# Kernel tuning notes

Hardware: AMD Instinct MI355X
Metric: run time of the kernel (lower is better)

## Reference

```python
import jax, jax.numpy as jnp
import numpy as np

EMBED = 256      # input_size
DOWN = 64        # expert hidden_size
NUM_EXPERTS = 10
TOPK = 2
GATE_SCALE = 0.5
LOSS_COEF = 1.0
CV_EPS = 1e-10


def setup_inputs() -> dict:
    key = jax.random.key(0)
    ks = jax.random.split(key, 6)
    B, N = 16, 4096
    x = jax.random.normal(ks[0], (B, N, EMBED), jnp.float32)
    # gating weight (Parameter in torch; random here so top-k is non-degenerate)
    w_gate = jax.random.normal(ks[1], (EMBED, NUM_EXPERTS), jnp.float32) * 0.02
    # expert MLP params: fc1 (EMBED->DOWN), relu, fc2 (DOWN->EMBED)
    w1 = jax.random.normal(ks[2], (NUM_EXPERTS, EMBED, DOWN), jnp.float32) * (1.0 / np.sqrt(EMBED))
    b1 = jnp.zeros((NUM_EXPERTS, DOWN), jnp.float32)
    w2 = jax.random.normal(ks[3], (NUM_EXPERTS, DOWN, EMBED), jnp.float32) * (1.0 / np.sqrt(DOWN))
    b2 = jnp.zeros((NUM_EXPERTS, EMBED), jnp.float32)
    return {"x": x, "w_gate": w_gate, "w1": w1, "b1": b1, "w2": w2, "b2": b2}


def _cv_squared(v):
    # torch: x.var() / (x.mean()**2 + eps), unbiased variance
    return jnp.var(v, ddof=1) / (jnp.mean(v) ** 2 + CV_EPS)


def reference(x, w_gate, w1, b1, w2, b2):
    B, N, D = x.shape
    xt = x.reshape(B * N, D)                      # (T, D)
    T = B * N

    # --- noisy top-k gating (eval mode: no noise) ---
    logits = xt @ w_gate                          # (T, E)
    top_logits, top_idx = jax.lax.top_k(logits, TOPK)
    top_gates = jax.nn.softmax(top_logits, axis=-1)
    gates = jnp.zeros((T, NUM_EXPERTS), x.dtype).at[
        jnp.arange(T)[:, None], top_idx].set(top_gates)   # (T, E), sparse rows

    importance = gates.sum(axis=0)                               # (E,)
    load = jnp.sum(gates > 0, axis=0).astype(x.dtype)            # (E,)
    aux_loss = (_cv_squared(importance) + _cv_squared(load)) * LOSS_COEF

    # --- expert FFN dispatch+combine (dense equivalent: zero gates kill terms) ---
    h = jax.nn.relu(jnp.einsum('td,edh->teh', xt, w1) + b1[None])   # (T, E, DOWN)
    ye = jnp.einsum('teh,eho->teo', h, w2) + b2[None]               # (T, E, D)
    y = jnp.einsum('te,teo->to', gates, ye)                         # (T, D)

    out = y.reshape(B, N, -1)
    # self-KD L1 loss vs zeros, computed BEFORE gate_scale is applied
    kd_loss = jnp.mean(jnp.abs(out))
    moe_loss = aux_loss + kd_loss
    return out * GATE_SCALE, moe_loss
```

## Files before the change

kernel.cpp:

```cpp
#include <hip/hip_runtime.h>
#include <hip/hip_bf16.h>

#define T_TOKENS 65536
#define EMBED 256
#define DOWN 64
#define NE 10
#define TILE 64
#define XROW 72

typedef __attribute__((ext_vector_type(8))) short short8;
typedef __attribute__((ext_vector_type(4))) float f32x4;

__device__ inline unsigned short f2bf(float f) {
    unsigned u = __builtin_bit_cast(unsigned, f);
    u += 0x7fff + ((u >> 16) & 1);
    return (unsigned short)(u >> 16);
}
__device__ inline float bf2f(unsigned short h) {
    unsigned u = ((unsigned)h) << 16;
    return __builtin_bit_cast(float, u);
}

__global__ __launch_bounds__(256) void pack_kernel(
    const float* __restrict__ w1, const float* __restrict__ w2,
    unsigned short* __restrict__ w1ph, unsigned short* __restrict__ w1pl,
    unsigned short* __restrict__ w2ph, unsigned short* __restrict__ w2pl)
{
    int gid = blockIdx.x * 256 + threadIdx.x;
    int lane = gid & 63;
    int fid = gid >> 6;
    int n16 = lane & 15;
    int kbase = ((lane >> 4) & 3) * 8;
    if (fid < 320) {
        int kb = fid & 7, ect = fid >> 3;
        int ct = ect & 3, e = ect >> 2;
        int n = ct * 16 + n16;
        int k0 = kb * 32 + kbase;
#pragma unroll
        for (int j = 0; j < 8; ++j) {
            float v = w1[((size_t)e * EMBED + k0 + j) * DOWN + n];
            unsigned short h = f2bf(v);
            w1ph[(size_t)fid * 512 + lane * 8 + j] = h;
            w1pl[(size_t)fid * 512 + lane * 8 + j] = f2bf(v - bf2f(h));
        }
    } else if (fid < 640) {
        int f2 = fid - 320;
        int kb = f2 & 1, ect = f2 >> 1;
        int ct = ect & 15, e = ect >> 4;
        int n = ct * 16 + n16;
        int k0 = kb * 32 + kbase;
#pragma unroll
        for (int j = 0; j < 8; ++j) {
            float v = w2[((size_t)e * DOWN + k0 + j) * EMBED + n];
            unsigned short h = f2bf(v);
            w2ph[(size_t)f2 * 512 + lane * 8 + j] = h;
            w2pl[(size_t)f2 * 512 + lane * 8 + j] = f2bf(v - bf2f(h));
        }
    }
}

__global__ __launch_bounds__(256) void gating_kernel(
    const float* __restrict__ x, const float* __restrict__ wg,
    int* __restrict__ counts, float* __restrict__ importance,
    int* __restrict__ tok_list, float* __restrict__ gate_list)
{
    __shared__ int lcount[NE];
    __shared__ float limp[NE];
    __shared__ int gbase[NE];
    int tid = threadIdx.x;
    if (tid < NE) { lcount[tid] = 0; limp[tid] = 0.f; }
    __syncthreads();

    int t = blockIdx.x * 256 + tid;
    float acc[NE];
#pragma unroll
    for (int e = 0; e < NE; e++) acc[e] = 0.f;
    const float4* x4 = (const float4*)(x + (size_t)t * EMBED);
    for (int d4 = 0; d4 < EMBED / 4; d4++) {
        float4 xv = x4[d4];
        const float* xs = (const float*)&xv;
#pragma unroll
        for (int j = 0; j < 4; j++) {
            int d = d4 * 4 + j;
#pragma unroll
            for (int e = 0; e < NE; e++)
                acc[e] = fmaf(xs[j], wg[d * NE + e], acc[e]);
        }
    }
    float l0 = -INFINITY, l1 = -INFINITY;
    int i0 = 0, i1 = 0;
#pragma unroll
    for (int e = 0; e < NE; e++) {
        float v = acc[e];
        if (v > l0) { l1 = l0; i1 = i0; l0 = v; i0 = e; }
        else if (v > l1) { l1 = v; i1 = e; }
    }
    float ex = __expf(l1 - l0);
    float g0 = 1.f / (1.f + ex);
    float g1 = ex * g0;

    int lp0 = atomicAdd(&lcount[i0], 1);
    int lp1 = atomicAdd(&lcount[i1], 1);
    atomicAdd(&limp[i0], g0);
    atomicAdd(&limp[i1], g1);
    __syncthreads();
    if (tid < NE) {
        gbase[tid] = atomicAdd(&counts[tid], lcount[tid]);
        atomicAdd(&importance[tid], limp[tid]);
    }
    __syncthreads();
    int p0 = gbase[i0] + lp0;
    int p1 = gbase[i1] + lp1;
    tok_list[i0 * T_TOKENS + p0] = (t << 1) | 0;
    gate_list[i0 * T_TOKENS + p0] = g0;
    tok_list[i1 * T_TOKENS + p1] = (t << 1) | 1;
    gate_list[i1 * T_TOKENS + p1] = g1;
}

__global__ __launch_bounds__(256, 4) void expert_kernel(
    const float* __restrict__ x,
    const unsigned short* __restrict__ w1ph, const unsigned short* __restrict__ w1pl,
    const unsigned short* __restrict__ w2ph, const unsigned short* __restrict__ w2pl,
    const float* __restrict__ b1, const float* __restrict__ b2,
    const int* __restrict__ counts,
    const int* __restrict__ tok_list, const float* __restrict__ gate_list,
    float* __restrict__ y0, float* __restrict__ y1)
{
    int e = blockIdx.y;
    int cnt = counts[e];
    int start = blockIdx.x * TILE;
    if (start >= cnt) return;
    int m = min(TILE, cnt - start);

    __shared__ __align__(16) unsigned short Xh[TILE * XROW];
    __shared__ __align__(16) unsigned short Xl[TILE * XROW];
    __shared__ __align__(16) unsigned short Hh[TILE * XROW];
    __shared__ __align__(16) unsigned short Hl[TILE * XROW];
    __shared__ int toks[TILE];
    __shared__ float gval[TILE];

    int tid = threadIdx.x;
    if (tid < TILE) {
        int v = 0; float g = 0.f;
        if (tid < m) {
            v = tok_list[e * T_TOKENS + start + tid];
            g = gate_list[e * T_TOKENS + start + tid];
        }
        toks[tid] = v; gval[tid] = g;
    }
    __syncthreads();

    int lane = tid & 63;
    int wv = tid >> 6;
    int ln15 = lane & 15;
    int quad = lane >> 4;

    int srow = tid >> 2;
    int scol0 = (tid & 3) * 16;
    bool srow_ok = srow < m;
    const float* xrow = x + (size_t)(toks[srow] >> 1) * EMBED;

    f32x4 acc1[4];
#pragma unroll
    for (int rt = 0; rt < 4; ++rt) acc1[rt] = (f32x4){0.f, 0.f, 0.f, 0.f};

    const unsigned short* w1he = w1ph + (((size_t)e * 4 + wv) * 8) * 512;
    const unsigned short* w1le = w1pl + (((size_t)e * 4 + wv) * 8) * 512;

    for (int c = 0; c < 4; ++c) {
#pragma unroll
        for (int p = 0; p < 4; ++p) {
            int col = scol0 + p * 4;
            float4 v = make_float4(0.f, 0.f, 0.f, 0.f);
            if (srow_ok) v = *(const float4*)(xrow + c * 64 + col);
            const float* vs = (const float*)&v;
            ushort4 hv, lv;
            unsigned short* hp = (unsigned short*)&hv;
            unsigned short* lp = (unsigned short*)&lv;
#pragma unroll
            for (int i = 0; i < 4; ++i) {
                unsigned short h = f2bf(vs[i]);
                hp[i] = h;
                lp[i] = f2bf(vs[i] - bf2f(h));
            }
            *(ushort4*)&Xh[srow * XROW + col] = hv;
            *(ushort4*)&Xl[srow * XROW + col] = lv;
        }
        __syncthreads();
#pragma unroll
        for (int kb = 0; kb < 2; ++kb) {
            int kbg = c * 2 + kb;
            short8 bh = *(const short8*)(w1he + (size_t)kbg * 512 + lane * 8);
            short8 bl = *(const short8*)(w1le + (size_t)kbg * 512 + lane * 8);
            int aoff = kb * 32 + quad * 8;
#pragma unroll
            for (int rt = 0; rt < 4; ++rt) {
                short8 ah = *(const short8*)&Xh[(rt * 16 + ln15) * XROW + aoff];
                short8 al = *(const short8*)&Xl[(rt * 16 + ln15) * XROW + aoff];
                acc1[rt] = __builtin_amdgcn_mfma_f32_16x16x32_bf16(ah, bh, acc1[rt], 0, 0, 0);
                acc1[rt] = __builtin_amdgcn_mfma_f32_16x16x32_bf16(ah, bl, acc1[rt], 0, 0, 0);
                acc1[rt] = __builtin_amdgcn_mfma_f32_16x16x32_bf16(al, bh, acc1[rt], 0, 0, 0);
            }
        }
        __syncthreads();
    }

    float b1v = b1[e * DOWN + wv * 16 + ln15];
#pragma unroll
    for (int rt = 0; rt < 4; ++rt) {
#pragma unroll
        for (int r = 0; r < 4; ++r) {
            float h = fmaxf(acc1[rt][r] + b1v, 0.f);
            unsigned short hh = f2bf(h);
            int row = rt * 16 + quad * 4 + r;
            Hh[row * XROW + wv * 16 + ln15] = hh;
            Hl[row * XROW + wv * 16 + ln15] = f2bf(h - bf2f(hh));
        }
    }
    __syncthreads();

    float b2v[4];
#pragma unroll
    for (int ci = 0; ci < 4; ++ci)
        b2v[ci] = b2[e * EMBED + (wv * 4 + ci) * 16 + ln15];

#pragma unroll
    for (int rt = 0; rt < 4; ++rt) {
        short8 ah[2], al[2];
#pragma unroll
        for (int kb = 0; kb < 2; ++kb) {
            int aoff = kb * 32 + quad * 8;
            ah[kb] = *(const short8*)&Hh[(rt * 16 + ln15) * XROW + aoff];
            al[kb] = *(const short8*)&Hl[(rt * 16 + ln15) * XROW + aoff];
        }
        int rowbase = rt * 16 + quad * 4;
#pragma unroll
        for (int ci = 0; ci < 4; ++ci) {
            int ct = wv * 4 + ci;
            const unsigned short* p2h = w2ph + (((size_t)e * 16 + ct) * 2) * 512;
            const unsigned short* p2l = w2pl + (((size_t)e * 16 + ct) * 2) * 512;
            f32x4 acc = (f32x4){0.f, 0.f, 0.f, 0.f};
#pragma unroll
            for (int kb = 0; kb < 2; ++kb) {
                short8 bh = *(const short8*)(p2h + kb * 512 + lane * 8);
                short8 bl = *(const short8*)(p2l + kb * 512 + lane * 8);
                acc = __builtin_amdgcn_mfma_f32_16x16x32_bf16(ah[kb], bh, acc, 0, 0, 0);
                acc = __builtin_amdgcn_mfma_f32_16x16x32_bf16(ah[kb], bl, acc, 0, 0, 0);
                acc = __builtin_amdgcn_mfma_f32_16x16x32_bf16(al[kb], bh, acc, 0, 0, 0);
            }
#pragma unroll
            for (int r = 0; r < 4; ++r) {
                int row = rowbase + r;
                if (row < m) {
                    int packed = toks[row];
                    float g = gval[row];
                    float val = g * (acc[r] + b2v[ci]);
                    float* dst = (packed & 1) ? y1 : y0;
                    dst[(size_t)(packed >> 1) * EMBED + ct * 16 + ln15] = val;
                }
            }
        }
    }
}

__global__ __launch_bounds__(256) void combine_kernel(
    float* __restrict__ out, const float* __restrict__ y1buf, float* __restrict__ kdpart)
{
    size_t idx = (size_t)blockIdx.x * 256 + threadIdx.x;
    float4 a = ((const float4*)out)[idx];
    float4 b = ((const float4*)y1buf)[idx];
    float4 v;
    v.x = a.x + b.x; v.y = a.y + b.y; v.z = a.z + b.z; v.w = a.w + b.w;
    float s = fabsf(v.x) + fabsf(v.y) + fabsf(v.z) + fabsf(v.w);
    v.x *= 0.5f; v.y *= 0.5f; v.z *= 0.5f; v.w *= 0.5f;
    ((float4*)out)[idx] = v;
#pragma unroll
    for (int o = 32; o > 0; o >>= 1) s += __shfl_down(s, o, 64);
    __shared__ float red[4];
    int lane = threadIdx.x & 63, wid = threadIdx.x >> 6;
    if (lane == 0) red[wid] = s;
    __syncthreads();
    if (threadIdx.x == 0) {
        float tot = red[0] + red[1] + red[2] + red[3];
        atomicAdd(&kdpart[blockIdx.x & 63], tot);
    }
}

__global__ void loss_kernel(const int* __restrict__ counts, const float* __restrict__ importance,
                            const float* __restrict__ kdpart, float* __restrict__ loss_out)
{
    if (threadIdx.x == 0) {
        float kd = 0.f;
        for (int i = 0; i < 64; i++) kd += kdpart[i];
        kd *= (1.f / (float)((size_t)T_TOKENS * EMBED));
        float mi = 0.f, ml = 0.f;
        for (int e = 0; e < NE; e++) { mi += importance[e]; ml += (float)counts[e]; }
        mi *= (1.f / NE); ml *= (1.f / NE);
        float vi = 0.f, vl = 0.f;
        for (int e = 0; e < NE; e++) {
            float di = importance[e] - mi; vi += di * di;
            float dl = (float)counts[e] - ml; vl += dl * dl;
        }
        vi *= (1.f / (NE - 1)); vl *= (1.f / (NE - 1));
        float aux = vi / (mi * mi + 1e-10f) + vl / (ml * ml + 1e-10f);
        loss_out[0] = aux + kd;
    }
}

extern "C" void kernel_launch(void* const* d_in, const int* in_sizes, int n_in,
                              void* d_out, int out_size, void* d_ws, size_t ws_size,
                              hipStream_t stream)
{
    (void)in_sizes; (void)n_in; (void)out_size; (void)ws_size;
    const float* x  = (const float*)d_in[0];
    const float* wg = (const float*)d_in[1];
    const float* w1 = (const float*)d_in[2];
    const float* b1 = (const float*)d_in[3];
    const float* w2 = (const float*)d_in[4];
    const float* b2 = (const float*)d_in[5];
    float* out = (float*)d_out;

    char* ws = (char*)d_ws;
    int*   counts     = (int*)ws;
    float* importance = (float*)(ws + 64);
    float* kdpart     = (float*)(ws + 128);
    size_t off = 512;
    int*   tok_list   = (int*)(ws + off);   off += (size_t)NE * T_TOKENS * 4;
    float* gate_list  = (float*)(ws + off); off += (size_t)NE * T_TOKENS * 4;
    unsigned short* w1ph = (unsigned short*)(ws + off); off += 327680;
    unsigned short* w1pl = (unsigned short*)(ws + off); off += 327680;
    unsigned short* w2ph = (unsigned short*)(ws + off); off += 327680;
    unsigned short* w2pl = (unsigned short*)(ws + off); off += 327680;
    float* y1buf = (float*)(ws + off);

    hipMemsetAsync(ws, 0, 512, stream);

    pack_kernel<<<160, 256, 0, stream>>>(w1, w2, w1ph, w1pl, w2ph, w2pl);
    gating_kernel<<<T_TOKENS / 256, 256, 0, stream>>>(x, wg, counts, importance, tok_list, gate_list);
    expert_kernel<<<dim3(T_TOKENS / TILE, NE), 256, 0, stream>>>(
        x, w1ph, w1pl, w2ph, w2pl, b1, b2, counts, tok_list, gate_list, out, y1buf);
    combine_kernel<<<(T_TOKENS * (EMBED / 4)) / 256, 256, 0, stream>>>(out, y1buf, kdpart);
    loss_kernel<<<1, 64, 0, stream>>>(counts, importance, kdpart, out + (size_t)T_TOKENS * EMBED);
}
```

Baseline: 264.6 us.

## Bucket tokens by expert pair and fuse combine into expert kernel

Gating now bins each token by its (top1, top2) expert pair, and a queue kernel builds a compact list of 64-token work tiles per pair. Each expert block computes both experts for its tokens, pre-scales the hidden activations by the gates, and sums both second-layer GEMMs into one accumulator. It then writes the final scaled output and the L1 partial sums directly, which removes the y1 buffer and the separate combine pass. Gating also stages x through shared memory to get coalesced loads. The cost is a serial single-thread queue build, a 100-bucket workspace, lower occupancy (launch bounds 3), and a fixed grid of 1114 blocks that must cover the queue length.

```diff
diff --git a/kernel.cpp b/kernel.cpp
--- a/kernel.cpp
+++ b/kernel.cpp
@@ -5,7 +5,8 @@
 #define EMBED 256
 #define DOWN 64
 #define NE 10
-#define TILE 64
+#define NPAIR 100
+#define MAXQ 1280
 #define XROW 72
 
 typedef __attribute__((ext_vector_type(8))) short short8;
@@ -61,32 +62,53 @@
 
 __global__ __launch_bounds__(256) void gating_kernel(
     const float* __restrict__ x, const float* __restrict__ wg,
-    int* __restrict__ counts, float* __restrict__ importance,
-    int* __restrict__ tok_list, float* __restrict__ gate_list)
-{
-    __shared__ int lcount[NE];
-    __shared__ float limp[NE];
-    __shared__ int gbase[NE];
+    int* __restrict__ pcount, float* __restrict__ importance,
+    int* __restrict__ btok, float* __restrict__ bg0)
+{
+    __shared__ float Xs[2][256 * 33];
+    __shared__ int lcount[NPAIR];
+    __shared__ int gbase[NPAIR];
+    __shared__ float limp[16];
     int tid = threadIdx.x;
-    if (tid < NE) { lcount[tid] = 0; limp[tid] = 0.f; }
-    __syncthreads();
-
-    int t = blockIdx.x * 256 + tid;
+    if (tid < NPAIR) lcount[tid] = 0;
+    if (tid < 16) limp[tid] = 0.f;
+
+    int tokbase = blockIdx.x * 256;
+    const float4* x4 = (const float4*)x;
+    int rbase = tid >> 3, c4 = tid & 7;
+
+    float4 pre[8];
+#pragma unroll
+    for (int i = 0; i < 8; ++i)
+        pre[i] = x4[(size_t)(tokbase + i * 32 + rbase) * 64 + c4];
+
     float acc[NE];
 #pragma unroll
     for (int e = 0; e < NE; e++) acc[e] = 0.f;
-    const float4* x4 = (const float4*)(x + (size_t)t * EMBED);
-    for (int d4 = 0; d4 < EMBED / 4; d4++) {
-        float4 xv = x4[d4];
-        const float* xs = (const float*)&xv;
-#pragma unroll
-        for (int j = 0; j < 4; j++) {
-            int d = d4 * 4 + j;
-#pragma unroll
-            for (int e = 0; e < NE; e++)
-                acc[e] = fmaf(xs[j], wg[d * NE + e], acc[e]);
-        }
-    }
+
+    for (int cc = 0; cc < 8; ++cc) {
+        float* buf = Xs[cc & 1];
+#pragma unroll
+        for (int i = 0; i < 8; ++i) {
+            float* d = &buf[(i * 32 + rbase) * 33 + c4 * 4];
+            d[0] = pre[i].x; d[1] = pre[i].y; d[2] = pre[i].z; d[3] = pre[i].w;
+        }
+        if (cc < 7) {
+#pragma unroll
+            for (int i = 0; i < 8; ++i)
+                pre[i] = x4[(size_t)(tokbase + i * 32 + rbase) * 64 + (cc + 1) * 8 + c4];
+        }
+        __syncthreads();
+        const float* wgc = wg + cc * 32 * NE;
+#pragma unroll
+        for (int c = 0; c < 32; ++c) {
+            float xv = buf[tid * 33 + c];
+#pragma unroll
+            for (int e = 0; e < NE; ++e)
+                acc[e] = fmaf(xv, wgc[c * NE + e], acc[e]);
+        }
+    }
+
     float l0 = -INFINITY, l1 = -INFINITY;
     int i0 = 0, i1 = 0;
 #pragma unroll
@@ -97,91 +119,102 @@
     }
     float ex = __expf(l1 - l0);
     float g0 = 1.f / (1.f + ex);
-    float g1 = ex * g0;
-
-    int lp0 = atomicAdd(&lcount[i0], 1);
-    int lp1 = atomicAdd(&lcount[i1], 1);
+
+    int p = i0 * NE + i1;
+    int lp = atomicAdd(&lcount[p], 1);
     atomicAdd(&limp[i0], g0);
-    atomicAdd(&limp[i1], g1);
-    __syncthreads();
-    if (tid < NE) {
-        gbase[tid] = atomicAdd(&counts[tid], lcount[tid]);
-        atomicAdd(&importance[tid], limp[tid]);
-    }
-    __syncthreads();
-    int p0 = gbase[i0] + lp0;
-    int p1 = gbase[i1] + lp1;
-    tok_list[i0 * T_TOKENS + p0] = (t << 1) | 0;
-    gate_list[i0 * T_TOKENS + p0] = g0;
-    tok_list[i1 * T_TOKENS + p1] = (t << 1) | 1;
-    gate_list[i1 * T_TOKENS + p1] = g1;
-}
-
-__global__ __launch_bounds__(256, 4) void expert_kernel(
+    atomicAdd(&limp[i1], 1.f - g0);
+    __syncthreads();
+    if (tid < NPAIR) {
+        int c = lcount[tid];
+        gbase[tid] = c ? atomicAdd(&pcount[tid], c) : 0;
+    }
+    if (tid < NE) atomicAdd(&importance[tid], limp[tid]);
+    __syncthreads();
+    int pos = gbase[p] + lp;
+    btok[p * T_TOKENS + pos] = tokbase + tid;
+    bg0[p * T_TOKENS + pos] = g0;
+}
+
+__global__ void queue_kernel(const int* __restrict__ pcount,
+                             int* __restrict__ qp, int* __restrict__ qs, int* __restrict__ nq)
+{
+    if (threadIdx.x == 0) {
+        int n = 0;
+        for (int p = 0; p < NPAIR; p++) {
+            int c = pcount[p];
+            for (int s = 0; s < c; s += 64) { qp[n] = p; qs[n] = s; n++; }
+        }
+        *nq = n;
+    }
+}
+
+__global__ __launch_bounds__(256, 3) void expert_kernel(
     const float* __restrict__ x,
     const unsigned short* __restrict__ w1ph, const unsigned short* __restrict__ w1pl,
     const unsigned short* __restrict__ w2ph, const unsigned short* __restrict__ w2pl,
     const float* __restrict__ b1, const float* __restrict__ b2,
-    const int* __restrict__ counts,
-    const int* __restrict__ tok_list, const float* __restrict__ gate_list,
-    float* __restrict__ y0, float* __restrict__ y1)
-{
-    int e = blockIdx.y;
-    int cnt = counts[e];
-    int start = blockIdx.x * TILE;
-    if (start >= cnt) return;
-    int m = min(TILE, cnt - start);
-
-    __shared__ __align__(16) unsigned short Xh[TILE * XROW];
-    __shared__ __align__(16) unsigned short Xl[TILE * XROW];
-    __shared__ __align__(16) unsigned short Hh[TILE * XROW];
-    __shared__ __align__(16) unsigned short Hl[TILE * XROW];
-    __shared__ int toks[TILE];
-    __shared__ float gval[TILE];
+    const int* __restrict__ pcount, const int* __restrict__ qp, const int* __restrict__ qs,
+    const int* __restrict__ nq,
+    const int* __restrict__ btok, const float* __restrict__ bg0,
+    float* __restrict__ out, float* __restrict__ kdpart)
+{
+    int bid = blockIdx.x;
+    if (bid >= *nq) return;
+    int p = qp[bid], s = qs[bid];
+    int e0 = p / NE, e1 = p - e0 * NE;
+    int m = min(64, pcount[p] - s);
+
+    __shared__ __align__(16) unsigned short Xh[64 * XROW], Xl[64 * XROW];
+    __shared__ __align__(16) unsigned short H0h[4096], H0l[4096];
+    __shared__ __align__(16) unsigned short H1h[4096], H1l[4096];
+    __shared__ int toks[64];
+    __shared__ float gv0s[64], gv1s[64];
+    __shared__ float kdw[4];
 
     int tid = threadIdx.x;
-    if (tid < TILE) {
+    if (tid < 64) {
         int v = 0; float g = 0.f;
         if (tid < m) {
-            v = tok_list[e * T_TOKENS + start + tid];
-            g = gate_list[e * T_TOKENS + start + tid];
-        }
-        toks[tid] = v; gval[tid] = g;
-    }
-    __syncthreads();
-
-    int lane = tid & 63;
-    int wv = tid >> 6;
-    int ln15 = lane & 15;
-    int quad = lane >> 4;
-
-    int srow = tid >> 2;
-    int scol0 = (tid & 3) * 16;
+            v = btok[p * T_TOKENS + s + tid];
+            g = bg0[p * T_TOKENS + s + tid];
+        }
+        toks[tid] = v;
+        gv0s[tid] = g;
+        gv1s[tid] = (tid < m) ? (1.f - g) : 0.f;
+    }
+    __syncthreads();
+
+    int lane = tid & 63, wv = tid >> 6;
+    int ln15 = lane & 15, quad = lane >> 4;
+    int srow = tid >> 2, sc0 = (tid & 3) * 16;
+    const float* xrow = x + (size_t)toks[srow] * EMBED;
     bool srow_ok = srow < m;
-    const float* xrow = x + (size_t)(toks[srow] >> 1) * EMBED;
-
-    f32x4 acc1[4];
-#pragma unroll
-    for (int rt = 0; rt < 4; ++rt) acc1[rt] = (f32x4){0.f, 0.f, 0.f, 0.f};
-
-    const unsigned short* w1he = w1ph + (((size_t)e * 4 + wv) * 8) * 512;
-    const unsigned short* w1le = w1pl + (((size_t)e * 4 + wv) * 8) * 512;
-
-    for (int c = 0; c < 4; ++c) {
-#pragma unroll
-        for (int p = 0; p < 4; ++p) {
-            int col = scol0 + p * 4;
+
+    f32x4 a10[4], a11[4];
+#pragma unroll
+    for (int rt = 0; rt < 4; ++rt) { a10[rt] = (f32x4){0,0,0,0}; a11[rt] = (f32x4){0,0,0,0}; }
+
+    const unsigned short* w1h0 = w1ph + (((size_t)e0 * 4 + wv) * 8) * 512;
+    const unsigned short* w1l0 = w1pl + (((size_t)e0 * 4 + wv) * 8) * 512;
+    const unsigned short* w1h1 = w1ph + (((size_t)e1 * 4 + wv) * 8) * 512;
+    const unsigned short* w1l1 = w1pl + (((size_t)e1 * 4 + wv) * 8) * 512;
+
+    for (int cc = 0; cc < 4; ++cc) {
+#pragma unroll
+        for (int p4 = 0; p4 < 4; ++p4) {
+            int col = sc0 + p4 * 4;
             float4 v = make_float4(0.f, 0.f, 0.f, 0.f);
-            if (srow_ok) v = *(const float4*)(xrow + c * 64 + col);
+            if (srow_ok) v = *(const float4*)(xrow + cc * 64 + col);
             const float* vs = (const float*)&v;
             ushort4 hv, lv;
             unsigned short* hp = (unsigned short*)&hv;
-            unsigned short* lp = (unsigned short*)&lv;
+            unsigned short* lp2 = (unsigned short*)&lv;
 #pragma unroll
             for (int i = 0; i < 4; ++i) {
                 unsigned short h = f2bf(vs[i]);
                 hp[i] = h;
-                lp[i] = f2bf(vs[i] - bf2f(h));
+                lp2[i] = f2bf(vs[i] - bf2f(h));
             }
             *(ushort4*)&Xh[srow * XROW + col] = hv;
             *(ushort4*)&Xl[srow * XROW + col] = lv;
@@ -189,117 +222,134 @@
         __syncthreads();
 #pragma unroll
         for (int kb = 0; kb < 2; ++kb) {
-            int kbg = c * 2 + kb;
-            short8 bh = *(const short8*)(w1he + (size_t)kbg * 512 + lane * 8);
-            short8 bl = *(const short8*)(w1le + (size_t)kbg * 512 + lane * 8);
+            int kbg = cc * 2 + kb;
+            short8 bh0 = *(const short8*)(w1h0 + (size_t)kbg * 512 + lane * 8);
+            short8 bl0 = *(const short8*)(w1l0 + (size_t)kbg * 512 + lane * 8);
+            short8 bh1 = *(const short8*)(w1h1 + (size_t)kbg * 512 + lane * 8);
+            short8 bl1 = *(const short8*)(w1l1 + (size_t)kbg * 512 + lane * 8);
             int aoff = kb * 32 + quad * 8;
 #pragma unroll
             for (int rt = 0; rt < 4; ++rt) {
                 short8 ah = *(const short8*)&Xh[(rt * 16 + ln15) * XROW + aoff];
                 short8 al = *(const short8*)&Xl[(rt * 16 + ln15) * XROW + aoff];
-                acc1[rt] = __builtin_amdgcn_mfma_f32_16x16x32_bf16(ah, bh, acc1[rt], 0, 0, 0);
-                acc1[rt] = __builtin_amdgcn_mfma_f32_16x16x32_bf16(ah, bl, acc1[rt], 0, 0, 0);
-                acc1[rt] = __builtin_amdgcn_mfma_f32_16x16x32_bf16(al, bh, acc1[rt], 0, 0, 0);
+                a10[rt] = __builtin_amdgcn_mfma_f32_16x16x32_bf16(ah, bh0, a10[rt], 0, 0, 0);
+                a10[rt] = __builtin_amdgcn_mfma_f32_16x16x32_bf16(ah, bl0, a10[rt], 0, 0, 0);
+                a10[rt] = __builtin_amdgcn_mfma_f32_16x16x32_bf16(al, bh0, a10[rt], 0, 0, 0);
+                a11[rt] = __builtin_amdgcn_mfma_f32_16x16x32_bf16(ah, bh1, a11[rt], 0, 0, 0);
+                a11[rt] = __builtin_amdgcn_mfma_f32_16x16x32_bf16(ah, bl1, a11[rt], 0, 0, 0);
+                a11[rt] = __builtin_amdgcn_mfma_f32_16x16x32_bf16(al, bh1, a11[rt], 0, 0, 0);
             }
         }
         __syncthreads();
     }
 
-    float b1v = b1[e * DOWN + wv * 16 + ln15];
+    {
+        float b1v0 = b1[e0 * DOWN + wv * 16 + ln15];
+        float b1v1 = b1[e1 * DOWN + wv * 16 + ln15];
+        int kbH = wv >> 1;
+        int laneH = (((wv & 1) * 2 + (ln15 >> 3)) * 16) + quad * 4;
+        int jH = ln15 & 7;
+#pragma unroll
+        for (int rt = 0; rt < 4; ++rt) {
+#pragma unroll
+            for (int r = 0; r < 4; ++r) {
+                int row = rt * 16 + quad * 4 + r;
+                float g0 = gv0s[row], g1 = gv1s[row];
+                float h0 = fmaxf(a10[rt][r] + b1v0, 0.f) * g0;
+                float h1 = fmaxf(a11[rt][r] + b1v1, 0.f) * g1;
+                int idx = ((rt * 2 + kbH) * 64 + laneH + r) * 8 + jH;
+                unsigned short h0h = f2bf(h0);
+                unsigned short h1h = f2bf(h1);
+                H0h[idx] = h0h; H0l[idx] = f2bf(h0 - bf2f(h0h));
+                H1h[idx] = h1h; H1l[idx] = f2bf(h1 - bf2f(h1h));
+            }
+        }
+    }
+    __syncthreads();
+
+    float b20[4], b21[4];
+#pragma unroll
+    for (int ci = 0; ci < 4; ++ci) {
+        b20[ci] = b2[e0 * EMBED + (wv * 4 + ci) * 16 + ln15];
+        b21[ci] = b2[e1 * EMBED + (wv * 4 + ci) * 16 + ln15];
+    }
+    float kdacc = 0.f;
 #pragma unroll
     for (int rt = 0; rt < 4; ++rt) {
-#pragma unroll
-        for (int r = 0; r < 4; ++r) {
-            float h = fmaxf(acc1[rt][r] + b1v, 0.f);
-            unsigned short hh = f2bf(h);
-            int row = rt * 16 + quad * 4 + r;
-            Hh[row * XROW + wv * 16 + ln15] = hh;
-            Hl[row * XROW + wv * 16 + ln15] = f2bf(h - bf2f(hh));
-        }
-    }
-    __syncthreads();
-
-    float b2v[4];
-#pragma unroll
-    for (int ci = 0; ci < 4; ++ci)
-        b2v[ci] = b2[e * EMBED + (wv * 4 + ci) * 16 + ln15];
-
-#pragma unroll
-    for (int rt = 0; rt < 4; ++rt) {
-        short8 ah[2], al[2];
+        short8 ah0[2], al0[2], ah1[2], al1[2];
 #pragma unroll
         for (int kb = 0; kb < 2; ++kb) {
-            int aoff = kb * 32 + quad * 8;
-            ah[kb] = *(const short8*)&Hh[(rt * 16 + ln15) * XROW + aoff];
-            al[kb] = *(const short8*)&Hl[(rt * 16 + ln15) * XROW + aoff];
-        }
-        int rowbase = rt * 16 + quad * 4;
+            int base = ((rt * 2 + kb) * 64 + lane) * 8;
+            ah0[kb] = *(const short8*)&H0h[base];
+            al0[kb] = *(const short8*)&H0l[base];
+            ah1[kb] = *(const short8*)&H1h[base];
+            al1[kb] = *(const short8*)&H1l[base];
+        }
+        int rowb = rt * 16 + quad * 4;
+        float gr0[4], gr1[4];
+#pragma unroll
+        for (int r = 0; r < 4; ++r) { gr0[r] = gv0s[rowb + r]; gr1[r] = gv1s[rowb + r]; }
 #pragma unroll
         for (int ci = 0; ci < 4; ++ci) {
             int ct = wv * 4 + ci;
-            const unsigned short* p2h = w2ph + (((size_t)e * 16 + ct) * 2) * 512;
-            const unsigned short* p2l = w2pl + (((size_t)e * 16 + ct) * 2) * 512;
-            f32x4 acc = (f32x4){0.f, 0.f, 0.f, 0.f};
+            const unsigned short* p0h = w2ph + (((size_t)e0 * 16 + ct) * 2) * 512;
+            const unsigned short* p0l = w2pl + (((size_t)e0 * 16 + ct) * 2) * 512;
+            const unsigned short* p1h = w2ph + (((size_t)e1 * 16 + ct) * 2) * 512;
+            const unsigned short* p1l = w2pl + (((size_t)e1 * 16 + ct) * 2) * 512;
+            f32x4 acc = (f32x4){0, 0, 0, 0};
 #pragma unroll
             for (int kb = 0; kb < 2; ++kb) {
-                short8 bh = *(const short8*)(p2h + kb * 512 + lane * 8);
-                short8 bl = *(const short8*)(p2l + kb * 512 + lane * 8);
-                acc = __builtin_amdgcn_mfma_f32_16x16x32_bf16(ah[kb], bh, acc, 0, 0, 0);
-                acc = __builtin_amdgcn_mfma_f32_16x16x32_bf16(ah[kb], bl, acc, 0, 0, 0);
-                acc = __builtin_amdgcn_mfma_f32_16x16x32_bf16(al[kb], bh, acc, 0, 0, 0);
+                short8 bh = *(const short8*)(p0h + kb * 512 + lane * 8);
+                short8 bl = *(const short8*)(p0l + kb * 512 + lane * 8);
+                acc = __builtin_amdgcn_mfma_f32_16x16x32_bf16(ah0[kb], bh, acc, 0, 0, 0);
+                acc = __builtin_amdgcn_mfma_f32_16x16x32_bf16(ah0[kb], bl, acc, 0, 0, 0);
+                acc = __builtin_amdgcn_mfma_f32_16x16x32_bf16(al0[kb], bh, acc, 0, 0, 0);
+                short8 ch = *(const short8*)(p1h + kb * 512 + lane * 8);
+                short8 cl = *(const short8*)(p1l + kb * 512 + lane * 8);
+                acc = __builtin_amdgcn_mfma_f32_16x16x32_bf16(ah1[kb], ch, acc, 0, 0, 0);
+                acc = __builtin_amdgcn_mfma_f32_16x16x32_bf16(ah1[kb], cl, acc, 0, 0, 0);
+                acc = __builtin_amdgcn_mfma_f32_16x16x32_bf16(al1[kb], ch, acc, 0, 0, 0);
             }
 #pragma unroll
             for (int r = 0; r < 4; ++r) {
-                int row = rowbase + r;
+                int row = rowb + r;
+                float val = acc[r] + gr0[r] * b20[ci] + gr1[r] * b21[ci];
                 if (row < m) {
-                    int packed = toks[row];
-                    float g = gval[row];
-                    float val = g * (acc[r] + b2v[ci]);
-                    float* dst = (packed & 1) ? y1 : y0;
-                    dst[(size_t)(packed >> 1) * EMBED + ct * 16 + ln15] = val;
+                    kdacc += fabsf(val);
+                    out[(size_t)toks[row] * EMBED + ct * 16 + ln15] = 0.5f * val;
                 }
             }
         }
     }
-}
-
-__global__ __launch_bounds__(256) void combine_kernel(
-    float* __restrict__ out, const float* __restrict__ y1buf, float* __restrict__ kdpart)
-{
-    size_t idx = (size_t)blockIdx.x * 256 + threadIdx.x;
-    float4 a = ((const float4*)out)[idx];
-    float4 b = ((const float4*)y1buf)[idx];
-    float4 v;
-    v.x = a.x + b.x; v.y = a.y + b.y; v.z = a.z + b.z; v.w = a.w + b.w;
-    float s = fabsf(v.x) + fabsf(v.y) + fabsf(v.z) + fabsf(v.w);
-    v.x *= 0.5f; v.y *= 0.5f; v.z *= 0.5f; v.w *= 0.5f;
-    ((float4*)out)[idx] = v;
-#pragma unroll
-    for (int o = 32; o > 0; o >>= 1) s += __shfl_down(s, o, 64);
-    __shared__ float red[4];
-    int lane = threadIdx.x & 63, wid = threadIdx.x >> 6;
-    if (lane == 0) red[wid] = s;
-    __syncthreads();
-    if (threadIdx.x == 0) {
-        float tot = red[0] + red[1] + red[2] + red[3];
-        atomicAdd(&kdpart[blockIdx.x & 63], tot);
-    }
-}
-
-__global__ void loss_kernel(const int* __restrict__ counts, const float* __restrict__ importance,
+#pragma unroll
+    for (int o = 32; o > 0; o >>= 1) kdacc += __shfl_down(kdacc, o, 64);
+    if (lane == 0) kdw[wv] = kdacc;
+    __syncthreads();
+    if (tid == 0)
+        atomicAdd(&kdpart[bid & 63], kdw[0] + kdw[1] + kdw[2] + kdw[3]);
+}
+
+__global__ void loss_kernel(const int* __restrict__ pcount, const float* __restrict__ importance,
                             const float* __restrict__ kdpart, float* __restrict__ loss_out)
 {
     if (threadIdx.x == 0) {
         float kd = 0.f;
         for (int i = 0; i < 64; i++) kd += kdpart[i];
         kd *= (1.f / (float)((size_t)T_TOKENS * EMBED));
+        float load[NE];
+        for (int e = 0; e < NE; e++) load[e] = 0.f;
+        for (int p = 0; p < NPAIR; p++) {
+            float c = (float)pcount[p];
+            load[p / NE] += c;
+            load[p % NE] += c;
+        }
         float mi = 0.f, ml = 0.f;
-        for (int e = 0; e < NE; e++) { mi += importance[e]; ml += (float)counts[e]; }
+        for (int e = 0; e < NE; e++) { mi += importance[e]; ml += load[e]; }
         mi *= (1.f / NE); ml *= (1.f / NE);
         float vi = 0.f, vl = 0.f;
         for (int e = 0; e < NE; e++) {
             float di = importance[e] - mi; vi += di * di;
-            float dl = (float)counts[e] - ml; vl += dl * dl;
+            float dl = load[e] - ml; vl += dl * dl;
         }
         vi *= (1.f / (NE - 1)); vl *= (1.f / (NE - 1));
         float aux = vi / (mi * mi + 1e-10f) + vl / (ml * ml + 1e-10f);
@@ -321,24 +371,26 @@
     float* out = (float*)d_out;
 
     char* ws = (char*)d_ws;
-    int*   counts     = (int*)ws;
-    float* importance = (float*)(ws + 64);
-    float* kdpart     = (float*)(ws + 128);
-    size_t off = 512;
-    int*   tok_list   = (int*)(ws + off);   off += (size_t)NE * T_TOKENS * 4;
-    float* gate_list  = (float*)(ws + off); off += (size_t)NE * T_TOKENS * 4;
+    int*   pcount     = (int*)ws;
+    float* importance = (float*)(ws + 512);
+    float* kdpart     = (float*)(ws + 576);
+    int*   nq         = (int*)(ws + 832);
+    int*   qp         = (int*)(ws + 1024);
+    int*   qs         = (int*)(ws + 1024 + MAXQ * 4);
+    size_t off = 16384;
+    int*   btok = (int*)(ws + off);    off += (size_t)NPAIR * T_TOKENS * 4;
+    float* bg0  = (float*)(ws + off);  off += (size_t)NPAIR * T_TOKENS * 4;
     unsigned short* w1ph = (unsigned short*)(ws + off); off += 327680;
     unsigned short* w1pl = (unsigned short*)(ws + off); off += 327680;
     unsigned short* w2ph = (unsigned short*)(ws + off); off += 327680;
     unsigned short* w2pl = (unsigned short*)(ws + off); off += 327680;
-    float* y1buf = (float*)(ws + off);
-
-    hipMemsetAsync(ws, 0, 512, stream);
+
+    hipMemsetAsync(ws, 0, 1024, stream);
 
     pack_kernel<<<160, 256, 0, stream>>>(w1, w2, w1ph, w1pl, w2ph, w2pl);
-    gating_kernel<<<T_TOKENS / 256, 256, 0, stream>>>(x, wg, counts, importance, tok_list, gate_list);
-    expert_kernel<<<dim3(T_TOKENS / TILE, NE), 256, 0, stream>>>(
-        x, w1ph, w1pl, w2ph, w2pl, b1, b2, counts, tok_list, gate_list, out, y1buf);
-    combine_kernel<<<(T_TOKENS * (EMBED / 4)) / 256, 256, 0, stream>>>(out, y1buf, kdpart);
-    loss_kernel<<<1, 64, 0, stream>>>(counts, importance, kdpart, out + (size_t)T_TOKENS * EMBED);
-}
+    gating_kernel<<<T_TOKENS / 256, 256, 0, stream>>>(x, wg, pcount, importance, btok, bg0);
+    queue_kernel<<<1, 64, 0, stream>>>(pcount, qp, qs, nq);
+    expert_kernel<<<1114, 256, 0, stream>>>(
+        x, w1ph, w1pl, w2ph, w2pl, b1, b2, pcount, qp, qs, nq, btok, bg0, out, kdpart);
+    loss_kernel<<<1, 64, 0, stream>>>(pcount, importance, kdpart, out + (size_t)T_TOKENS * EMBED);
+}
```

After: 261.0 us. About the same (-1.4%).
